# Optimization experiments

Measured on AMD Instinct MI355X. Metric: run time of the kernel, lower is better.

The kernel has to match this reference:

```python
import jax, jax.numpy as jnp
import numpy as np

N, E, B = 50000, 800000, 64
F0, H, C = 8, 2, 64          # node feat dim, heads, per-head out dim
OBS, MH, NA = 128, 256, 16   # obs dim, mlp hidden, n_actions
NEG_SLOPE = 0.2


def setup_inputs() -> dict:
    key = jax.random.key(0)
    ks = jax.random.split(key, 30)
    p = lambda k, shape: (jax.random.normal(k, shape, dtype=jnp.float32) * 0.1)
    inp = {
        "obs": jax.random.normal(ks[0], (B, OBS), dtype=jnp.float32),
        "node_features": jax.random.normal(ks[1], (N, F0), dtype=jnp.float32),
        "edge_index": jax.random.randint(ks[2], (2, E), 0, N, dtype=jnp.int32),
        "batch": jnp.sort(jax.random.randint(ks[3], (N,), 0, B, dtype=jnp.int32)),
        # GAT layer 0: in=F0 -> heads=H, out=C, concat
        "W0": p(ks[4], (F0, H * C)), "a_src0": p(ks[5], (H, C)), "a_dst0": p(ks[6], (H, C)), "b0": p(ks[7], (H * C,)),
        # GAT layer 1: in=H*C -> heads=H, out=C, concat
        "W1": p(ks[8], (H * C, H * C)), "a_src1": p(ks[9], (H, C)), "a_dst1": p(ks[10], (H, C)), "b1": p(ks[11], (H * C,)),
        # GAT layer 2: in=H*C -> heads=1, out=C, no concat
        "W2": p(ks[12], (H * C, C)), "a_src2": p(ks[13], (1, C)), "a_dst2": p(ks[14], (1, C)), "b2": p(ks[15], (C,)),
        # MLP head: combined = C + OBS
        "Ws1": p(ks[16], (C + OBS, MH)), "bs1": p(ks[17], (MH,)),
        "ln_g": jnp.ones((MH,), jnp.float32), "ln_b": jnp.zeros((MH,), jnp.float32),
        "Ws2": p(ks[18], (MH, MH)), "bs2": p(ks[19], (MH,)),
        "Wa": p(ks[20], (MH, NA)), "ba": p(ks[21], (NA,)),
        "Wc": p(ks[22], (MH, 1)), "bc": p(ks[23], (1,)),
    }
    return inp


def gat_layer(x, src, dst, W, a_src, a_dst, bias, heads, out_dim, concat):
    n = x.shape[0]
    h = (x @ W).reshape(n, heads, out_dim)                     # [N,H,C]
    alpha_s = jnp.einsum("nhc,hc->nh", h, a_src)               # [N,H]
    alpha_d = jnp.einsum("nhc,hc->nh", h, a_dst)
    e = jax.nn.leaky_relu(alpha_s[src] + alpha_d[dst], NEG_SLOPE)  # [E,H]
    # scatter-softmax over incoming edges of each dst node (stable)
    emax = jax.ops.segment_max(e, dst, num_segments=n)
    ex = jnp.exp(e - emax[dst])
    denom = jax.ops.segment_sum(ex, dst, num_segments=n)
    alpha = ex / (denom[dst] + 1e-16)                          # [E,H]
    msg = h[src] * alpha[..., None]                            # [E,H,C]
    out = jax.ops.segment_sum(msg, dst, num_segments=n)        # [N,H,C]
    out = out.reshape(n, heads * out_dim) if concat else out.mean(axis=1)
    return out + bias


def reference(obs, node_features, edge_index, batch,
              W0, a_src0, a_dst0, b0, W1, a_src1, a_dst1, b1,
              W2, a_src2, a_dst2, b2,
              Ws1, bs1, ln_g, ln_b, Ws2, bs2, Wa, ba, Wc, bc):
    n = node_features.shape[0]
    # PyG GATConv default add_self_loops=True
    loop = jnp.arange(n, dtype=edge_index.dtype)
    src = jnp.concatenate([edge_index[0], loop])
    dst = jnp.concatenate([edge_index[1], loop])

    x = node_features
    x = jax.nn.elu(gat_layer(x, src, dst, W0, a_src0, a_dst0, b0, H, C, True))
    x = jax.nn.elu(gat_layer(x, src, dst, W1, a_src1, a_dst1, b1, H, C, True))
    x = gat_layer(x, src, dst, W2, a_src2, a_dst2, b2, 1, C, False)

    # global mean pool over graphs
    counts = jax.ops.segment_sum(jnp.ones((n,), x.dtype), batch, num_segments=B)
    pooled = jax.ops.segment_sum(x, batch, num_segments=B) / jnp.maximum(counts, 1.0)[:, None]

    combined = jnp.concatenate([pooled, obs], axis=-1)         # [B, C+OBS]
    h = combined @ Ws1 + bs1
    mu = h.mean(-1, keepdims=True)
    var = ((h - mu) ** 2).mean(-1, keepdims=True)
    h = (h - mu) / jnp.sqrt(var + 1e-5) * ln_g + ln_b
    h = jax.nn.relu(h)
    h = jax.nn.relu(h @ Ws2 + bs2)
    logits = h @ Wa + ba
    value = (h @ Wc + bc).squeeze(-1)
    return logits, value
```

## Files before the change

kernel.cpp:

```cpp
#include <hip/hip_runtime.h>
#include <math.h>


#define LRELU(x) ((x) > 0.f ? (x) : 0.2f * (x))

typedef short bf16x8 __attribute__((ext_vector_type(8)));
typedef unsigned short u16x8 __attribute__((ext_vector_type(8)));
typedef float f32x4 __attribute__((ext_vector_type(4)));
typedef float f32x2 __attribute__((ext_vector_type(2)));

__device__ __forceinline__ float readlane_f(float v, int lane) {
    return __int_as_float(__builtin_amdgcn_readlane(__float_as_int(v), lane));
}
__device__ __forceinline__ unsigned readlane_u(unsigned v, int lane) {
    return (unsigned)__builtin_amdgcn_readlane((int)v, lane);
}
__device__ __forceinline__ unsigned short f2bf(float f) {
    unsigned int u = __float_as_uint(f);
    u = (u + 0x7fffu + ((u >> 16) & 1u)) >> 16;
    return (unsigned short)u;
}
__device__ __forceinline__ float bf2f(unsigned short u) {
    return __uint_as_float((unsigned int)u << 16);
}
__device__ __forceinline__ unsigned char f2fp8(float f) {
    return (unsigned char)(__builtin_amdgcn_cvt_pk_fp8_f32(f, f, 0, false) & 0xff);
}
__device__ __forceinline__ f32x2 fp8pair(unsigned int u) {
    return __builtin_amdgcn_cvt_pk_f32_fp8(u, false);
}


__global__ __launch_bounds__(256) void hist_t0_kernel(
    const int* __restrict__ dst, int* __restrict__ histT,
    int e, int G1, int NB, int n, int hist_blocks, int t0_blocks, int wp_blocks,
    const float* __restrict__ x, const float* __restrict__ W,
    const float* __restrict__ a_src, const float* __restrict__ a_dst,
    unsigned char* __restrict__ h, float* __restrict__ as_o,
    float* __restrict__ ad_o,
    const float* __restrict__ W1, const float* __restrict__ W2,
    unsigned short* __restrict__ Wf1, unsigned short* __restrict__ Wf2,
    const int* __restrict__ batch, int* __restrict__ gstart, int nGraphs) {
    __shared__ unsigned int hist[256];
    __shared__ float xs[2][8][8];
    if ((int)blockIdx.x < hist_blocks) {
        hist[threadIdx.x] = 0;
        __syncthreads();
        int base = blockIdx.x * 2048 + threadIdx.x * 8;
        int d[8];
        if (base + 8 <= e) {
            int4 x0 = *(const int4*)(dst + base);
            int4 x1 = *(const int4*)(dst + base + 4);
            d[0] = x0.x; d[1] = x0.y; d[2] = x0.z; d[3] = x0.w;
            d[4] = x1.x; d[5] = x1.y; d[6] = x1.z; d[7] = x1.w;
        } else {
#pragma unroll
            for (int j = 0; j < 8; j++) {
                int ij = base + j;
                d[j] = (ij < e) ? dst[ij] : -1;
            }
        }
#pragma unroll
        for (int j = 0; j < 8; j++) {
            if (d[j] >= 0) atomicAdd(&hist[d[j] >> 8], 1u);
        }
        __syncthreads();
        int b = threadIdx.x;
        if (b < NB) histT[b * G1 + blockIdx.x] = (int)hist[b];
        return;
    }
    if ((int)blockIdx.x < hist_blocks + t0_blocks) {
        const int bid2 = blockIdx.x - hist_blocks;
        const int tid = threadIdx.x & 127;
        const int half = threadIdx.x >> 7;
        const int node0 = bid2 * 16 + half * 8;

        for (int idx = tid; idx < 64; idx += 128) {
            int ni = idx >> 3, k = idx & 7;
            int ng = node0 + ni;
            xs[half][ni][k] = (ng < n) ? x[(size_t)ng * 8 + k] : 0.f;
        }
        __syncthreads();

        float acc[8];
#pragma unroll
        for (int i = 0; i < 8; i++) acc[i] = 0.f;
#pragma unroll
        for (int k = 0; k < 8; k++) {
            float wk = W[k * 128 + tid];
#pragma unroll
            for (int i = 0; i < 8; i++) acc[i] += xs[half][i][k] * wk;
        }

        const int lane = tid & 63;
        const int head = tid >> 6;
        const int pos = 2 * lane + head;
        const float av = a_src[tid];
        const float dv = a_dst[tid];
#pragma unroll
        for (int i = 0; i < 8; i++) {
            int ng = node0 + i;
            if (ng >= n) break;
            h[(size_t)ng * 128 + pos] = f2fp8(acc[i]);
            float ps = acc[i] * av, pd = acc[i] * dv;
            for (int off = 32; off; off >>= 1) {
                ps += __shfl_xor(ps, off, 64);
                pd += __shfl_xor(pd, off, 64);
            }
            if (lane == 0) {
                as_o[ng * 2 + head] = ps;
                ad_o[ng * 2 + head] = pd;
            }
        }
        return;
    }
    if ((int)blockIdx.x < hist_blocks + t0_blocks + wp_blocks) {
        const int n1 = 8 * 4 * 64;
        const int n2 = 4 * 4 * 64;
        int gid = (blockIdx.x - hist_blocks - t0_blocks) * 256 + threadIdx.x;
        if (gid < n1) {
            int idx = gid;
            int lane = idx & 63, ts = idx >> 6;
            int s = ts & 3, t = ts >> 2;
            int quad = lane >> 4, cn = lane & 15;
#pragma unroll
            for (int j = 0; j < 8; j++)
                Wf1[idx * 8 + j] = f2bf(W1[(s * 32 + quad * 8 + j) * 128 + t * 16 + cn]);
        } else if (gid < n1 + n2) {
            int idx = gid - n1;
            int lane = idx & 63, ts = idx >> 6;
            int s = ts & 3, t = ts >> 2;
            int quad = lane >> 4, cn = lane & 15;
#pragma unroll
            for (int j = 0; j < 8; j++)
                Wf2[idx * 8 + j] = f2bf(W2[(s * 32 + quad * 8 + j) * 64 + t * 16 + cn]);
        }
        return;
    }
    int gid = (blockIdx.x - hist_blocks - t0_blocks - wp_blocks) * 256 + threadIdx.x;
    if (gid < n) {
        int bi = batch[gid];
        if (gid == 0) {
            for (int g = 0; g <= bi; g++) gstart[g] = 0;
        } else {
            int bp = batch[gid - 1];
            if (bi != bp)
                for (int g = bp + 1; g <= bi; g++) gstart[g] = gid;
        }
        if (gid == n - 1) {
            for (int g = bi + 1; g <= nGraphs; g++) gstart[g] = n;
        }
    }
}


__global__ __launch_bounds__(256) void scan2_block_kernel(
    const int* __restrict__ in, int* __restrict__ out,
    int* __restrict__ blockSums, int len) {
    __shared__ int lds[256];
    int t = threadIdx.x;
    int i0 = blockIdx.x * 512 + 2 * t;
    int v0 = (i0 < len) ? in[i0] : 0;
    int v1 = (i0 + 1 < len) ? in[i0 + 1] : 0;
    int s = v0 + v1;
    lds[t] = s;
    __syncthreads();
    for (int off = 1; off < 256; off <<= 1) {
        int u = (t >= off) ? lds[t - off] : 0;
        __syncthreads();
        lds[t] += u;
        __syncthreads();
    }
    int base = lds[t] - s;
    if (i0 < len) out[i0] = base;
    if (i0 + 1 < len) out[i0 + 1] = base + v0;
    if (t == 255) blockSums[blockIdx.x] = lds[255];
}

__global__ __launch_bounds__(256) void scan2_finalize_kernel(
    int* __restrict__ out, const int* __restrict__ blockSums, int len, int nb) {
    __shared__ int lds[256];
    int t = threadIdx.x;
    int v = (t < nb) ? blockSums[t] : 0;
    lds[t] = v;
    __syncthreads();
    for (int off = 1; off < 256; off <<= 1) {
        int u = (t >= off) ? lds[t - off] : 0;
        __syncthreads();
        lds[t] += u;
        __syncthreads();
    }
    const int bid = blockIdx.x;
    const int base = (bid > 0) ? lds[bid - 1] : 0;
    const int total = lds[nb - 1];
    int i0 = bid * 512 + 2 * t;
#pragma unroll
    for (int q = 0; q < 2; q++) {
        int i = i0 + q;
        if (i < len) out[i] += base;
        else if (i == len) out[len] = total;
    }
}


__global__ __launch_bounds__(256) void bucket_scatter_kernel(
    const int* __restrict__ src, const int* __restrict__ dst,
    const int* __restrict__ offs, int* __restrict__ esrc,
    unsigned char* __restrict__ dsub8, int e, int G1) {
    __shared__ unsigned int hist[256];
    hist[threadIdx.x] = 0;
    __syncthreads();
    int base = blockIdx.x * 2048 + threadIdx.x * 8;
    int d[8], s[8];
    if (base + 8 <= e) {
        int4 d0 = *(const int4*)(dst + base);
        int4 d1 = *(const int4*)(dst + base + 4);
        int4 s0 = *(const int4*)(src + base);
        int4 s1 = *(const int4*)(src + base + 4);
        d[0] = d0.x; d[1] = d0.y; d[2] = d0.z; d[3] = d0.w;
        d[4] = d1.x; d[5] = d1.y; d[6] = d1.z; d[7] = d1.w;
        s[0] = s0.x; s[1] = s0.y; s[2] = s0.z; s[3] = s0.w;
        s[4] = s1.x; s[5] = s1.y; s[6] = s1.z; s[7] = s1.w;
    } else {
#pragma unroll
        for (int j = 0; j < 8; j++) {
            int ij = base + j;
            bool v = ij < e;
            d[j] = v ? dst[ij] : -1;
            s[j] = v ? src[ij] : 0;
        }
    }
    unsigned lr[8];
#pragma unroll
    for (int j = 0; j < 8; j++) {
        lr[j] = (d[j] >= 0) ? atomicAdd(&hist[d[j] >> 8], 1u) : 0u;
    }
#pragma unroll
    for (int j = 0; j < 8; j++) {
        if (d[j] >= 0) {
            int pos = offs[(d[j] >> 8) * G1 + blockIdx.x] + (int)lr[j];
            esrc[pos] = s[j];
            dsub8[pos] = (unsigned char)(d[j] & 255);
        }
    }
}


__global__ __launch_bounds__(256) void bucket_csr_kernel(
    const int* __restrict__ offs, const unsigned char* __restrict__ dsub8,
    const int* __restrict__ esrc, int* __restrict__ row_ptr,
    int* __restrict__ col, int G1, int n) {
    __shared__ unsigned int cnt[256];
    __shared__ int rp[256];
    int t = threadIdx.x;
    int b = blockIdx.x;
    cnt[t] = 0;
    __syncthreads();
    int bs = offs[b * G1];
    int be = offs[(b + 1) * G1];
    for (int i = bs + t; i < be; i += 256) {
        atomicAdd(&cnt[dsub8[i]], 1u);
    }
    __syncthreads();
    int v = (int)cnt[t];
    rp[t] = v;
    __syncthreads();
    for (int off = 1; off < 256; off <<= 1) {
        int u = (t >= off) ? rp[t - off] : 0;
        __syncthreads();
        rp[t] += u;
        __syncthreads();
    }
    int excl = rp[t] - v;
    int node = b * 256 + t;
    if (node <= n) row_ptr[node] = bs + excl;
    __syncthreads();
    cnt[t] = (unsigned)excl;
    __syncthreads();
    for (int i = bs + t; i < be; i += 256) {
        int sub = dsub8[i];
        unsigned r = atomicAdd(&cnt[sub], 1u);
        col[bs + (int)r] = esrc[i];
    }
}

template <int OUT, int HEADS>
__device__ __forceinline__ int hpos8(int c) {
    return (HEADS == 2) ? (2 * (c & 63) + (c >> 6)) : c;
}


template <int OUT, int HEADS>
__global__ __launch_bounds__(256) void transform_mfma_kernel(
    const unsigned short* __restrict__ xb, const unsigned short* __restrict__ Wf,
    const float* __restrict__ a_src, const float* __restrict__ a_dst,
    unsigned char* __restrict__ h, float* __restrict__ as_o, float* __restrict__ ad_o,
    int n) {
    constexpr int T = OUT / 16, S = 4;
    const int w = threadIdx.x >> 6, lane = threadIdx.x & 63;
    const int node0 = (blockIdx.x * 4 + w) * 16;
    if (node0 >= n) return;
    const int quad = lane >> 4, col = lane & 15;

    const int arow = node0 + col;
    const bool aok = arow < n;
    bf16x8 a[S];
    const unsigned short* xrow = xb + (size_t)arow * 128 + quad * 8;
#pragma unroll
    for (int s = 0; s < S; s++) {
        bf16x8 z = {0, 0, 0, 0, 0, 0, 0, 0};
        a[s] = aok ? *(const bf16x8*)(xrow + s * 32) : z;
    }

    f32x4 acc[T];
#pragma unroll
    for (int t = 0; t < T; t++) acc[t] = (f32x4){0.f, 0.f, 0.f, 0.f};

#pragma unroll
    for (int s = 0; s < S; s++) {
#pragma unroll
        for (int t = 0; t < T; t++) {
            bf16x8 b = *(const bf16x8*)(Wf + ((size_t)(t * S + s) * 64 + lane) * 8);
            acc[t] = __builtin_amdgcn_mfma_f32_16x16x32_bf16(a[s], b, acc[t], 0, 0, 0);
        }
    }

#pragma unroll
    for (int t = 0; t < T; t++) {
        int pos = hpos8<OUT, HEADS>(t * 16 + col);
#pragma unroll
        for (int r = 0; r < 4; r++) {
            int m = node0 + quad * 4 + r;
            if (m < n) h[(size_t)m * OUT + pos] = f2fp8(acc[t][r]);
        }
    }

#pragma unroll
    for (int r = 0; r < 4; r++) {
        float s0 = 0.f, s1 = 0.f, d0 = 0.f, d1 = 0.f;
#pragma unroll
        for (int t = 0; t < T; t++) {
            float av = a_src[t * 16 + col];
            float dv = a_dst[t * 16 + col];
            float v = acc[t][r];
            if (HEADS == 2 && t >= T / 2) { s1 += v * av; d1 += v * dv; }
            else                          { s0 += v * av; d0 += v * dv; }
        }
        for (int off = 8; off; off >>= 1) {
            s0 += __shfl_xor(s0, off, 64);
            d0 += __shfl_xor(d0, off, 64);
            if (HEADS == 2) {
                s1 += __shfl_xor(s1, off, 64);
                d1 += __shfl_xor(d1, off, 64);
            }
        }
        int m = node0 + quad * 4 + r;
        if (m < n) {
            if (HEADS == 2) {
                if (col == 0)      { as_o[m * 2] = s0;     ad_o[m * 2] = d0; }
                else if (col == 1) { as_o[m * 2 + 1] = s1; ad_o[m * 2 + 1] = d1; }
            } else {
                if (col == 0) { as_o[m] = s0; ad_o[m] = d0; }
            }
        }
    }
}


template <int ACT>
__global__ __launch_bounds__(256) void agg2_kernel(
    const int* __restrict__ row_ptr, const int* __restrict__ col,
    const unsigned char* __restrict__ h, const float2* __restrict__ as2,
    const float2* __restrict__ ad2, const float* __restrict__ bias,
    unsigned short* __restrict__ out, int n) {
    const int node = blockIdx.x * 4 + (threadIdx.x >> 6);
    const int lane = threadIdx.x & 63;
    if (node >= n) return;

    const int beg = row_ptr[node], end = row_ptr[node + 1];
    const float2 adv = ad2[node];
    const unsigned char* __restrict__ hb = h + 2 * lane;

    const float2 avs = as2[node];
    float w0s = __expf(LRELU(avs.x + adv.x));
    float w1s = __expf(LRELU(avs.y + adv.y));
    unsigned int us = *(const unsigned short*)(hb + ((size_t)node << 7));
    f32x2 hvs = fp8pair(us);
    float accL = w0s * hvs.x, accH = w1s * hvs.y;
    float den0 = w0s, den1 = w1s;

    for (int base = beg; base < end; base += 64) {
        int cnt = end - base;
        if (cnt > 64) cnt = 64;
        int s = 0;
        float w0 = 0.f, w1 = 0.f;
        if (lane < cnt) {
            s = col[base + lane];
            float2 av = as2[s];
            w0 = __expf(LRELU(av.x + adv.x));
            w1 = __expf(LRELU(av.y + adv.y));
        }
        float t0 = w0, t1 = w1;
        for (int off = 32; off; off >>= 1) {
            t0 += __shfl_xor(t0, off, 64);
            t1 += __shfl_xor(t1, off, 64);
        }
        den0 += t0;
        den1 += t1;

        unsigned soff = (unsigned)s << 7;
        for (int j = 0; j < cnt; j += 8) {
            unsigned o0 = readlane_u(soff, j);
            unsigned o1 = readlane_u(soff, j + 1);
            unsigned o2 = readlane_u(soff, j + 2);
            unsigned o3 = readlane_u(soff, j + 3);
            unsigned o4 = readlane_u(soff, j + 4);
            unsigned o5 = readlane_u(soff, j + 5);
            unsigned o6 = readlane_u(soff, j + 6);
            unsigned o7 = readlane_u(soff, j + 7);
            unsigned u0 = *(const unsigned short*)(hb + o0);
            unsigned u1 = *(const unsigned short*)(hb + o1);
            unsigned u2 = *(const unsigned short*)(hb + o2);
            unsigned u3 = *(const unsigned short*)(hb + o3);
            unsigned u4 = *(const unsigned short*)(hb + o4);
            unsigned u5 = *(const unsigned short*)(hb + o5);
            unsigned u6 = *(const unsigned short*)(hb + o6);
            unsigned u7 = *(const unsigned short*)(hb + o7);
            float a0 = readlane_f(w0, j),     a1 = readlane_f(w1, j);
            float b0 = readlane_f(w0, j + 1), b1 = readlane_f(w1, j + 1);
            float c0 = readlane_f(w0, j + 2), c1 = readlane_f(w1, j + 2);
            float d0 = readlane_f(w0, j + 3), d1 = readlane_f(w1, j + 3);
            float e0 = readlane_f(w0, j + 4), e1 = readlane_f(w1, j + 4);
            float f0 = readlane_f(w0, j + 5), f1 = readlane_f(w1, j + 5);
            float g0 = readlane_f(w0, j + 6), g1 = readlane_f(w1, j + 6);
            float i0 = readlane_f(w0, j + 7), i1 = readlane_f(w1, j + 7);
            f32x2 hA = fp8pair(u0);
            f32x2 hB = fp8pair(u1);
            f32x2 hC = fp8pair(u2);
            f32x2 hD = fp8pair(u3);
            f32x2 hE = fp8pair(u4);
            f32x2 hF = fp8pair(u5);
            f32x2 hG = fp8pair(u6);
            f32x2 hH = fp8pair(u7);
            accL += a0 * hA.x; accH += a1 * hA.y;
            accL += b0 * hB.x; accH += b1 * hB.y;
            accL += c0 * hC.x; accH += c1 * hC.y;
            accL += d0 * hD.x; accH += d1 * hD.y;
            accL += e0 * hE.x; accH += e1 * hE.y;
            accL += f0 * hF.x; accH += f1 * hF.y;
            accL += g0 * hG.x; accH += g1 * hG.y;
            accL += i0 * hH.x; accH += i1 * hH.y;
        }
    }

    float oL = accL / (den0 + 1e-16f) + bias[lane];
    float oH = accH / (den1 + 1e-16f) + bias[64 + lane];
    if (ACT) {
        oL = oL > 0.f ? oL : expm1f(oL);
        oH = oH > 0.f ? oH : expm1f(oH);
    }
    out[(size_t)node * 128 + lane] = f2bf(oL);
    out[(size_t)node * 128 + 64 + lane] = f2bf(oH);
}


__global__ __launch_bounds__(256) void agg1_kernel(
    const int* __restrict__ row_ptr, const int* __restrict__ col,
    const unsigned char* __restrict__ h, const float* __restrict__ as1,
    const float* __restrict__ ad1, const float* __restrict__ bias,
    unsigned short* __restrict__ out, int n) {
    const int node = blockIdx.x * 4 + (threadIdx.x >> 6);
    const int lane = threadIdx.x & 63;
    if (node >= n) return;

    const int beg = row_ptr[node], end = row_ptr[node + 1];
    const float adv = ad1[node];
    const unsigned char* __restrict__ hb = h + lane;

    float ws = __expf(LRELU(as1[node] + adv));
    float acc = ws * fp8pair((unsigned)hb[(size_t)node << 6]).x;
    float den = ws;

    for (int base = beg; base < end; base += 64) {
        int cnt = end - base;
        if (cnt > 64) cnt = 64;
        int s = 0;
        float w = 0.f;
        if (lane < cnt) {
            s = col[base + lane];
            w = __expf(LRELU(as1[s] + adv));
        }
        float t = w;
        for (int off = 32; off; off >>= 1) t += __shfl_xor(t, off, 64);
        den += t;

        unsigned soff = (unsigned)s << 6;
        for (int j = 0; j < cnt; j += 8) {
            unsigned o0 = readlane_u(soff, j);
            unsigned o1 = readlane_u(soff, j + 1);
            unsigned o2 = readlane_u(soff, j + 2);
            unsigned o3 = readlane_u(soff, j + 3);
            unsigned o4 = readlane_u(soff, j + 4);
            unsigned o5 = readlane_u(soff, j + 5);
            unsigned o6 = readlane_u(soff, j + 6);
            unsigned o7 = readlane_u(soff, j + 7);
            unsigned u0 = hb[o0];
            unsigned u1 = hb[o1];
            unsigned u2 = hb[o2];
            unsigned u3 = hb[o3];
            unsigned u4 = hb[o4];
            unsigned u5 = hb[o5];
            unsigned u6 = hb[o6];
            unsigned u7 = hb[o7];
            float wA = readlane_f(w, j);
            float wB = readlane_f(w, j + 1);
            float wC = readlane_f(w, j + 2);
            float wD = readlane_f(w, j + 3);
            float wE = readlane_f(w, j + 4);
            float wF = readlane_f(w, j + 5);
            float wG = readlane_f(w, j + 6);
            float wH = readlane_f(w, j + 7);
            acc += wA * fp8pair(u0).x;
            acc += wB * fp8pair(u1).x;
            acc += wC * fp8pair(u2).x;
            acc += wD * fp8pair(u3).x;
            acc += wE * fp8pair(u4).x;
            acc += wF * fp8pair(u5).x;
            acc += wG * fp8pair(u6).x;
            acc += wH * fp8pair(u7).x;
        }
    }

    out[(size_t)node * 64 + lane] = f2bf(acc / (den + 1e-16f) + bias[lane]);
}


__global__ __launch_bounds__(512) void mlp_kernel(
    const unsigned short* __restrict__ xbuf, const int* __restrict__ gstart,
    const float* __restrict__ obs,
    const float* __restrict__ Ws1, const float* __restrict__ bs1,
    const float* __restrict__ ln_g, const float* __restrict__ ln_b,
    const float* __restrict__ Ws2, const float* __restrict__ bs2,
    const float* __restrict__ Wa, const float* __restrict__ ba,
    const float* __restrict__ Wc, const float* __restrict__ bc,
    float* __restrict__ out_logits, float* __restrict__ out_value) {
    int b = blockIdx.x;
    int t = threadIdx.x;
    __shared__ float comb[192];
    __shared__ float red[512];
    __shared__ float red2[8][64];
    __shared__ float hs[256];

    const int gs = gstart[b];
    const int ge = gstart[b + 1];

    {
        const int w = t >> 6, lane = t & 63;
        const int rg = w * 8 + (lane >> 3);
        const int sub = lane & 7;
        float acc[8];
#pragma unroll
        for (int j = 0; j < 8; j++) acc[j] = 0.f;
        for (int i = gs + rg; i < ge; i += 64) {
            u16x8 v = *(const u16x8*)(xbuf + (size_t)i * 64 + sub * 8);
#pragma unroll
            for (int j = 0; j < 8; j++) acc[j] += bf2f(v[j]);
        }
#pragma unroll
        for (int off = 8; off <= 32; off <<= 1) {
#pragma unroll
            for (int j = 0; j < 8; j++) acc[j] += __shfl_xor(acc[j], off, 64);
        }
        if (lane < 8) {
#pragma unroll
            for (int j = 0; j < 8; j++) red2[w][lane * 8 + j] = acc[j];
        }
    }
    __syncthreads();
    {
        float cdiv = fmaxf((float)(ge - gs), 1.f);
        if (t < 64) {
            float s = 0.f;
#pragma unroll
            for (int w = 0; w < 8; w++) s += red2[w][t];
            comb[t] = s / cdiv;
        } else if (t < 192) {
            comb[t] = obs[b * 128 + (t - 64)];
        }
    }
    __syncthreads();

    const int t256 = t & 255;
    const int khalf = t >> 8;

    {
        float accA = 0.f, accB = 0.f;
        int k0 = khalf * 96;
#pragma unroll 4
        for (int k = k0; k < k0 + 96; k += 2) {
            accA += comb[k] * Ws1[k * 256 + t256];
            accB += comb[k + 1] * Ws1[(k + 1) * 256 + t256];
        }
        red[t] = accA + accB;
    }
    __syncthreads();
    float acc = 0.f;
    if (t < 256) acc = bs1[t] + red[t] + red[t + 256];
    __syncthreads();

    red[t] = (t < 256) ? acc : 0.f;
    __syncthreads();
    for (int off = 128; off; off >>= 1) {
        if (t < off) red[t] += red[t + off];
        __syncthreads();
    }
    float mu = red[0] / 256.f;
    __syncthreads();
    float d = acc - mu;
    red[t] = (t < 256) ? d * d : 0.f;
    __syncthreads();
    for (int off = 128; off; off >>= 1) {
        if (t < off) red[t] += red[t + off];
        __syncthreads();
    }
    float var = red[0] / 256.f;
    if (t < 256) {
        float hn = d * rsqrtf(var + 1e-5f) * ln_g[t] + ln_b[t];
        hs[t] = hn > 0.f ? hn : 0.f;
    }
    __syncthreads();

    {
        float a2A = 0.f, a2B = 0.f;
        int k0 = khalf * 128;
#pragma unroll 4
        for (int k = k0; k < k0 + 128; k += 2) {
            a2A += hs[k] * Ws2[k * 256 + t256];
            a2B += hs[k + 1] * Ws2[(k + 1) * 256 + t256];
        }
        red[t] = a2A + a2B;
    }
    __syncthreads();
    float acc2 = 0.f;
    if (t < 256) {
        acc2 = bs2[t] + red[t] + red[t + 256];
        acc2 = acc2 > 0.f ? acc2 : 0.f;
    }
    __syncthreads();
    if (t < 256) hs[t] = acc2;
    __syncthreads();

    {
        int o = t & 15, ck = t >> 4;
        float p = 0.f;
#pragma unroll
        for (int k = 0; k < 8; k++)
            p += hs[ck * 8 + k] * Wa[(ck * 8 + k) * 16 + o];
        red[t] = p;
    }
    __syncthreads();
    for (int off = 16; off >= 1; off >>= 1) {
        if ((t >> 4) < off) red[t] += red[t + off * 16];
        __syncthreads();
    }
    if (t < 16) out_logits[b * 16 + t] = red[t] + ba[t];
    __syncthreads();

    red[t] = (t < 256) ? hs[t] * Wc[t] : 0.f;
    __syncthreads();
    for (int off = 256; off; off >>= 1) {
        if (t < off) red[t] += red[t + off];
        __syncthreads();
    }
    if (t == 0) out_value[b] = red[0] + bc[0];
}


extern "C" void kernel_launch(void* const* d_in, const int* in_sizes, int n_in,
                              void* d_out, int out_size, void* d_ws, size_t ws_size,
                              hipStream_t stream) {
    const float* obs    = (const float*)d_in[0];
    const float* nf     = (const float*)d_in[1];
    const int*   ei     = (const int*)d_in[2];
    const int*   batch  = (const int*)d_in[3];
    const float* W0     = (const float*)d_in[4];
    const float* a_src0 = (const float*)d_in[5];
    const float* a_dst0 = (const float*)d_in[6];
    const float* b0     = (const float*)d_in[7];
    const float* W1     = (const float*)d_in[8];
    const float* a_src1 = (const float*)d_in[9];
    const float* a_dst1 = (const float*)d_in[10];
    const float* b1     = (const float*)d_in[11];
    const float* W2     = (const float*)d_in[12];
    const float* a_src2 = (const float*)d_in[13];
    const float* a_dst2 = (const float*)d_in[14];
    const float* b2     = (const float*)d_in[15];
    const float* Ws1    = (const float*)d_in[16];
    const float* bs1    = (const float*)d_in[17];
    const float* ln_g   = (const float*)d_in[18];
    const float* ln_b   = (const float*)d_in[19];
    const float* Ws2    = (const float*)d_in[20];
    const float* bs2    = (const float*)d_in[21];
    const float* Wa     = (const float*)d_in[22];
    const float* ba     = (const float*)d_in[23];
    const float* Wc     = (const float*)d_in[24];
    const float* bc     = (const float*)d_in[25];

    const int N = in_sizes[3];
    const int E = in_sizes[2] / 2;
    const int B = in_sizes[0] / 128;
    const int* src = ei;
    const int* dstp = ei + E;

    char* p = (char*)d_ws;
    auto alloc = [&](size_t bytes) -> void* {
        void* r = (void*)p;
        p += (bytes + 255) & ~(size_t)255;
        return r;
    };
    const int G1 = (E + 2047) / 2048;
    const int NB = (N + 255) >> 8;
    const int L  = NB * G1;
    int*   row_ptr   = (int*)alloc((size_t)(N + 1) * 4);
    int*   col       = (int*)alloc((size_t)E * 4);
    int*   esrc      = (int*)alloc((size_t)E * 4);
    unsigned char* dsub8 = (unsigned char*)alloc((size_t)E);
    int*   histT     = (int*)alloc((size_t)L * 4);
    int*   offs      = (int*)alloc((size_t)(L + 1) * 4);
    unsigned char* hbuf = (unsigned char*)alloc((size_t)N * 128);
    unsigned short* xb = (unsigned short*)alloc((size_t)N * 128 * 2);
    unsigned short* xbuf = (unsigned short*)alloc((size_t)N * 64 * 2);
    float* as_       = (float*)alloc((size_t)N * 2 * 4);
    float* ad_       = (float*)alloc((size_t)N * 2 * 4);
    unsigned short* Wf1 = (unsigned short*)alloc((size_t)8 * 4 * 64 * 8 * 2);
    unsigned short* Wf2 = (unsigned short*)alloc((size_t)4 * 4 * 64 * 8 * 2);
    int* gstart      = (int*)alloc((size_t)(B + 1) * 4);
    int* blockSums = (int*)xb;

    float* out_logits = (float*)d_out;
    float* out_value  = out_logits + (size_t)B * 16;

    int t0_blocks = (N + 15) / 16;
    int wp_blocks = (8 * 4 * 64 + 4 * 4 * 64 + 255) / 256;
    int gb_blocks = (N + 255) / 256;
    hist_t0_kernel<<<G1 + t0_blocks + wp_blocks + gb_blocks, 256, 0, stream>>>(
        dstp, histT, E, G1, NB, N, G1, t0_blocks, wp_blocks,
        nf, W0, a_src0, a_dst0, hbuf, as_, ad_,
        W1, W2, Wf1, Wf2, batch, gstart, B);

    int nbA = (L + 511) / 512;
    scan2_block_kernel<<<nbA, 256, 0, stream>>>(histT, offs, blockSums, L);
    scan2_finalize_kernel<<<(L + 1 + 511) / 512, 256, 0, stream>>>(offs, blockSums, L, nbA);

    bucket_scatter_kernel<<<G1, 256, 0, stream>>>(src, dstp, offs, esrc, dsub8, E, G1);
    bucket_csr_kernel<<<NB, 256, 0, stream>>>(offs, dsub8, esrc, row_ptr, col, G1, N);

    agg2_kernel<1><<<(N + 3) / 4, 256, 0, stream>>>(
        row_ptr, col, hbuf, (const float2*)as_, (const float2*)ad_, b0, xb, N);

    transform_mfma_kernel<128, 2><<<(N + 63) / 64, 256, 0, stream>>>(
        xb, Wf1, a_src1, a_dst1, hbuf, as_, ad_, N);
    agg2_kernel<1><<<(N + 3) / 4, 256, 0, stream>>>(
        row_ptr, col, hbuf, (const float2*)as_, (const float2*)ad_, b1, xb, N);

    transform_mfma_kernel<64, 1><<<(N + 63) / 64, 256, 0, stream>>>(
        xb, Wf2, a_src2, a_dst2, hbuf, as_, ad_, N);
    agg1_kernel<<<(N + 3) / 4, 256, 0, stream>>>(
        row_ptr, col, hbuf, as_, ad_, b2, xbuf, N);

    mlp_kernel<<<B, 512, 0, stream>>>(xbuf, gstart, obs, Ws1, bs1, ln_g, ln_b,
                                      Ws2, bs2, Wa, ba, Wc, bc,
                                      out_logits, out_value);
}
```

Baseline: 292.8 us.

## Process two nodes per wavefront in GAT aggregation with half-wave gathers

Both aggregation kernels now map one node to each 32-lane half of a wavefront instead of a full 64-lane wave. Each lane gathers wider chunks (4 fp8 bytes or 2 bytes), and neighbour offsets and weights go through LDS instead of readlane broadcasts. The intent is to use lanes better, given an average degree of about 16 where most of a 64-wide wave sat idle, and to widen the per-lane loads and stores. The cost is some divergence: both halves loop to the larger of the two degrees, and each chunk adds LDS traffic.

```diff
diff --git a/kernel.cpp b/kernel.cpp
--- a/kernel.cpp
+++ b/kernel.cpp
@@ -9,12 +9,6 @@
 typedef float f32x4 __attribute__((ext_vector_type(4)));
 typedef float f32x2 __attribute__((ext_vector_type(2)));
 
-__device__ __forceinline__ float readlane_f(float v, int lane) {
-    return __int_as_float(__builtin_amdgcn_readlane(__float_as_int(v), lane));
-}
-__device__ __forceinline__ unsigned readlane_u(unsigned v, int lane) {
-    return (unsigned)__builtin_amdgcn_readlane((int)v, lane);
-}
 __device__ __forceinline__ unsigned short f2bf(float f) {
     unsigned int u = __float_as_uint(f);
     u = (u + 0x7fffu + ((u >> 16) & 1u)) >> 16;
@@ -373,94 +367,101 @@
     const unsigned char* __restrict__ h, const float2* __restrict__ as2,
     const float2* __restrict__ ad2, const float* __restrict__ bias,
     unsigned short* __restrict__ out, int n) {
-    const int node = blockIdx.x * 4 + (threadIdx.x >> 6);
+    __shared__ float w0l[4][2][32], w1l[4][2][32];
+    __shared__ unsigned sofl[4][2][32];
+    const int w = threadIdx.x >> 6;
     const int lane = threadIdx.x & 63;
-    if (node >= n) return;
-
-    const int beg = row_ptr[node], end = row_ptr[node + 1];
-    const float2 adv = ad2[node];
-    const unsigned char* __restrict__ hb = h + 2 * lane;
-
-    const float2 avs = as2[node];
-    float w0s = __expf(LRELU(avs.x + adv.x));
-    float w1s = __expf(LRELU(avs.y + adv.y));
-    unsigned int us = *(const unsigned short*)(hb + ((size_t)node << 7));
-    f32x2 hvs = fp8pair(us);
-    float accL = w0s * hvs.x, accH = w1s * hvs.y;
-    float den0 = w0s, den1 = w1s;
-
-    for (int base = beg; base < end; base += 64) {
-        int cnt = end - base;
-        if (cnt > 64) cnt = 64;
-        int s = 0;
+    const int half = lane >> 5, l = lane & 31;
+    const int node = blockIdx.x * 8 + w * 2 + half;
+    const bool active = node < n;
+
+    int beg = 0, deg = 0;
+    float2 adv = make_float2(0.f, 0.f);
+    float den0 = 0.f, den1 = 0.f;
+    float a0 = 0.f, a1 = 0.f, a2 = 0.f, a3 = 0.f;
+    if (active) {
+        beg = row_ptr[node];
+        deg = row_ptr[node + 1] - beg;
+        adv = ad2[node];
+        float2 avs = as2[node];
+        float w0s = __expf(LRELU(avs.x + adv.x));
+        float w1s = __expf(LRELU(avs.y + adv.y));
+        unsigned us = *(const unsigned*)(h + ((size_t)node << 7) + 4 * l);
+        f32x2 p0 = fp8pair(us & 0xffffu);
+        f32x2 p1 = fp8pair(us >> 16);
+        a0 = w0s * p0.x; a1 = w1s * p0.y;
+        a2 = w0s * p1.x; a3 = w1s * p1.y;
+        den0 = w0s; den1 = w1s;
+    }
+    int dmax = deg;
+    for (int off = 32; off; off >>= 1) dmax = max(dmax, __shfl_xor(dmax, off, 64));
+
+    for (int base = 0; base < dmax; base += 32) {
+        int cnt = deg - base;
+        cnt = cnt < 0 ? 0 : (cnt > 32 ? 32 : cnt);
         float w0 = 0.f, w1 = 0.f;
-        if (lane < cnt) {
-            s = col[base + lane];
+        unsigned so = 0;
+        if (l < cnt) {
+            int s = col[beg + base + l];
             float2 av = as2[s];
             w0 = __expf(LRELU(av.x + adv.x));
             w1 = __expf(LRELU(av.y + adv.y));
+            so = (unsigned)s << 7;
         }
         float t0 = w0, t1 = w1;
-        for (int off = 32; off; off >>= 1) {
+        for (int off = 16; off; off >>= 1) {
             t0 += __shfl_xor(t0, off, 64);
             t1 += __shfl_xor(t1, off, 64);
         }
-        den0 += t0;
-        den1 += t1;
-
-        unsigned soff = (unsigned)s << 7;
-        for (int j = 0; j < cnt; j += 8) {
-            unsigned o0 = readlane_u(soff, j);
-            unsigned o1 = readlane_u(soff, j + 1);
-            unsigned o2 = readlane_u(soff, j + 2);
-            unsigned o3 = readlane_u(soff, j + 3);
-            unsigned o4 = readlane_u(soff, j + 4);
-            unsigned o5 = readlane_u(soff, j + 5);
-            unsigned o6 = readlane_u(soff, j + 6);
-            unsigned o7 = readlane_u(soff, j + 7);
-            unsigned u0 = *(const unsigned short*)(hb + o0);
-            unsigned u1 = *(const unsigned short*)(hb + o1);
-            unsigned u2 = *(const unsigned short*)(hb + o2);
-            unsigned u3 = *(const unsigned short*)(hb + o3);
-            unsigned u4 = *(const unsigned short*)(hb + o4);
-            unsigned u5 = *(const unsigned short*)(hb + o5);
-            unsigned u6 = *(const unsigned short*)(hb + o6);
-            unsigned u7 = *(const unsigned short*)(hb + o7);
-            float a0 = readlane_f(w0, j),     a1 = readlane_f(w1, j);
-            float b0 = readlane_f(w0, j + 1), b1 = readlane_f(w1, j + 1);
-            float c0 = readlane_f(w0, j + 2), c1 = readlane_f(w1, j + 2);
-            float d0 = readlane_f(w0, j + 3), d1 = readlane_f(w1, j + 3);
-            float e0 = readlane_f(w0, j + 4), e1 = readlane_f(w1, j + 4);
-            float f0 = readlane_f(w0, j + 5), f1 = readlane_f(w1, j + 5);
-            float g0 = readlane_f(w0, j + 6), g1 = readlane_f(w1, j + 6);
-            float i0 = readlane_f(w0, j + 7), i1 = readlane_f(w1, j + 7);
-            f32x2 hA = fp8pair(u0);
-            f32x2 hB = fp8pair(u1);
-            f32x2 hC = fp8pair(u2);
-            f32x2 hD = fp8pair(u3);
-            f32x2 hE = fp8pair(u4);
-            f32x2 hF = fp8pair(u5);
-            f32x2 hG = fp8pair(u6);
-            f32x2 hH = fp8pair(u7);
-            accL += a0 * hA.x; accH += a1 * hA.y;
-            accL += b0 * hB.x; accH += b1 * hB.y;
-            accL += c0 * hC.x; accH += c1 * hC.y;
-            accL += d0 * hD.x; accH += d1 * hD.y;
-            accL += e0 * hE.x; accH += e1 * hE.y;
-            accL += f0 * hF.x; accH += f1 * hF.y;
-            accL += g0 * hG.x; accH += g1 * hG.y;
-            accL += i0 * hH.x; accH += i1 * hH.y;
-        }
-    }
-
-    float oL = accL / (den0 + 1e-16f) + bias[lane];
-    float oH = accH / (den1 + 1e-16f) + bias[64 + lane];
-    if (ACT) {
-        oL = oL > 0.f ? oL : expm1f(oL);
-        oH = oH > 0.f ? oH : expm1f(oH);
-    }
-    out[(size_t)node * 128 + lane] = f2bf(oL);
-    out[(size_t)node * 128 + 64 + lane] = f2bf(oH);
+        den0 += t0; den1 += t1;
+        w0l[w][half][l] = w0;
+        w1l[w][half][l] = w1;
+        sofl[w][half][l] = so;
+
+        int jmax = dmax - base;
+        jmax = jmax > 32 ? 32 : jmax;
+        for (int j = 0; j < jmax; j += 8) {
+            unsigned u[8];
+#pragma unroll
+            for (int k = 0; k < 8; k++) {
+                unsigned so_k = sofl[w][half][j + k];
+                u[k] = *(const unsigned*)(h + so_k + 4 * l);
+            }
+            float W0[8], W1[8];
+#pragma unroll
+            for (int k = 0; k < 8; k++) {
+                W0[k] = w0l[w][half][j + k];
+                W1[k] = w1l[w][half][j + k];
+            }
+#pragma unroll
+            for (int k = 0; k < 8; k++) {
+                f32x2 p0 = fp8pair(u[k] & 0xffffu);
+                f32x2 p1 = fp8pair(u[k] >> 16);
+                a0 += W0[k] * p0.x; a1 += W1[k] * p0.y;
+                a2 += W0[k] * p1.x; a3 += W1[k] * p1.y;
+            }
+        }
+    }
+
+    if (active) {
+        float2 bA = *(const float2*)(bias + 2 * l);
+        float2 bB = *(const float2*)(bias + 64 + 2 * l);
+        float r0 = 1.f / (den0 + 1e-16f), r1 = 1.f / (den1 + 1e-16f);
+        float o0 = a0 * r0 + bA.x;
+        float o1 = a1 * r1 + bB.x;
+        float o2 = a2 * r0 + bA.y;
+        float o3 = a3 * r1 + bB.y;
+        if (ACT) {
+            o0 = o0 > 0.f ? o0 : expm1f(o0);
+            o1 = o1 > 0.f ? o1 : expm1f(o1);
+            o2 = o2 > 0.f ? o2 : expm1f(o2);
+            o3 = o3 > 0.f ? o3 : expm1f(o3);
+        }
+        unsigned h0 = (unsigned)f2bf(o0) | ((unsigned)f2bf(o2) << 16);
+        unsigned h1 = (unsigned)f2bf(o1) | ((unsigned)f2bf(o3) << 16);
+        *(unsigned*)(out + (size_t)node * 128 + 2 * l) = h0;
+        *(unsigned*)(out + (size_t)node * 128 + 64 + 2 * l) = h1;
+    }
 }
 
 
@@ -469,69 +470,75 @@
     const unsigned char* __restrict__ h, const float* __restrict__ as1,
     const float* __restrict__ ad1, const float* __restrict__ bias,
     unsigned short* __restrict__ out, int n) {
-    const int node = blockIdx.x * 4 + (threadIdx.x >> 6);
+    __shared__ float wl[4][2][32];
+    __shared__ unsigned sofl[4][2][32];
+    const int w = threadIdx.x >> 6;
     const int lane = threadIdx.x & 63;
-    if (node >= n) return;
-
-    const int beg = row_ptr[node], end = row_ptr[node + 1];
-    const float adv = ad1[node];
-    const unsigned char* __restrict__ hb = h + lane;
-
-    float ws = __expf(LRELU(as1[node] + adv));
-    float acc = ws * fp8pair((unsigned)hb[(size_t)node << 6]).x;
-    float den = ws;
-
-    for (int base = beg; base < end; base += 64) {
-        int cnt = end - base;
-        if (cnt > 64) cnt = 64;
-        int s = 0;
-        float w = 0.f;
-        if (lane < cnt) {
-            s = col[base + lane];
-            w = __expf(LRELU(as1[s] + adv));
-        }
-        float t = w;
-        for (int off = 32; off; off >>= 1) t += __shfl_xor(t, off, 64);
+    const int half = lane >> 5, l = lane & 31;
+    const int node = blockIdx.x * 8 + w * 2 + half;
+    const bool active = node < n;
+
+    int beg = 0, deg = 0;
+    float adv = 0.f, den = 0.f, a0 = 0.f, a2 = 0.f;
+    if (active) {
+        beg = row_ptr[node];
+        deg = row_ptr[node + 1] - beg;
+        adv = ad1[node];
+        float ws = __expf(LRELU(as1[node] + adv));
+        unsigned us = *(const unsigned short*)(h + ((size_t)node << 6) + 2 * l);
+        f32x2 p = fp8pair(us);
+        a0 = ws * p.x;
+        a2 = ws * p.y;
+        den = ws;
+    }
+    int dmax = deg;
+    for (int off = 32; off; off >>= 1) dmax = max(dmax, __shfl_xor(dmax, off, 64));
+
+    for (int base = 0; base < dmax; base += 32) {
+        int cnt = deg - base;
+        cnt = cnt < 0 ? 0 : (cnt > 32 ? 32 : cnt);
+        float w0 = 0.f;
+        unsigned so = 0;
+        if (l < cnt) {
+            int s = col[beg + base + l];
+            w0 = __expf(LRELU(as1[s] + adv));
+            so = (unsigned)s << 6;
+        }
+        float t = w0;
+        for (int off = 16; off; off >>= 1) t += __shfl_xor(t, off, 64);
         den += t;
-
-        unsigned soff = (unsigned)s << 6;
-        for (int j = 0; j < cnt; j += 8) {
-            unsigned o0 = readlane_u(soff, j);
-            unsigned o1 = readlane_u(soff, j + 1);
-            unsigned o2 = readlane_u(soff, j + 2);
-            unsigned o3 = readlane_u(soff, j + 3);
-            unsigned o4 = readlane_u(soff, j + 4);
-            unsigned o5 = readlane_u(soff, j + 5);
-            unsigned o6 = readlane_u(soff, j + 6);
-            unsigned o7 = readlane_u(soff, j + 7);
-            unsigned u0 = hb[o0];
-            unsigned u1 = hb[o1];
-            unsigned u2 = hb[o2];
-            unsigned u3 = hb[o3];
-            unsigned u4 = hb[o4];
-            unsigned u5 = hb[o5];
-            unsigned u6 = hb[o6];
-            unsigned u7 = hb[o7];
-            float wA = readlane_f(w, j);
-            float wB = readlane_f(w, j + 1);
-            float wC = readlane_f(w, j + 2);
-            float wD = readlane_f(w, j + 3);
-            float wE = readlane_f(w, j + 4);
-            float wF = readlane_f(w, j + 5);
-            float wG = readlane_f(w, j + 6);
-            float wH = readlane_f(w, j + 7);
-            acc += wA * fp8pair(u0).x;
-            acc += wB * fp8pair(u1).x;
-            acc += wC * fp8pair(u2).x;
-            acc += wD * fp8pair(u3).x;
-            acc += wE * fp8pair(u4).x;
-            acc += wF * fp8pair(u5).x;
-            acc += wG * fp8pair(u6).x;
-            acc += wH * fp8pair(u7).x;
-        }
-    }
-
-    out[(size_t)node * 64 + lane] = f2bf(acc / (den + 1e-16f) + bias[lane]);
+        wl[w][half][l] = w0;
+        sofl[w][half][l] = so;
+
+        int jmax = dmax - base;
+        jmax = jmax > 32 ? 32 : jmax;
+        for (int j = 0; j < jmax; j += 8) {
+            unsigned u[8];
+#pragma unroll
+            for (int k = 0; k < 8; k++) {
+                unsigned so_k = sofl[w][half][j + k];
+                u[k] = *(const unsigned short*)(h + so_k + 2 * l);
+            }
+            float W0[8];
+#pragma unroll
+            for (int k = 0; k < 8; k++) W0[k] = wl[w][half][j + k];
+#pragma unroll
+            for (int k = 0; k < 8; k++) {
+                f32x2 p = fp8pair(u[k]);
+                a0 += W0[k] * p.x;
+                a2 += W0[k] * p.y;
+            }
+        }
+    }
+
+    if (active) {
+        float2 bA = *(const float2*)(bias + 2 * l);
+        float r = 1.f / (den + 1e-16f);
+        float o0 = a0 * r + bA.x;
+        float o2 = a2 * r + bA.y;
+        unsigned hv = (unsigned)f2bf(o0) | ((unsigned)f2bf(o2) << 16);
+        *(unsigned*)(out + (size_t)node * 64 + 2 * l) = hv;
+    }
 }
 
 
@@ -755,17 +762,17 @@
     bucket_scatter_kernel<<<G1, 256, 0, stream>>>(src, dstp, offs, esrc, dsub8, E, G1);
     bucket_csr_kernel<<<NB, 256, 0, stream>>>(offs, dsub8, esrc, row_ptr, col, G1, N);
 
-    agg2_kernel<1><<<(N + 3) / 4, 256, 0, stream>>>(
+    agg2_kernel<1><<<(N + 7) / 8, 256, 0, stream>>>(
         row_ptr, col, hbuf, (const float2*)as_, (const float2*)ad_, b0, xb, N);
 
     transform_mfma_kernel<128, 2><<<(N + 63) / 64, 256, 0, stream>>>(
         xb, Wf1, a_src1, a_dst1, hbuf, as_, ad_, N);
-    agg2_kernel<1><<<(N + 3) / 4, 256, 0, stream>>>(
+    agg2_kernel<1><<<(N + 7) / 8, 256, 0, stream>>>(
         row_ptr, col, hbuf, (const float2*)as_, (const float2*)ad_, b1, xb, N);
 
     transform_mfma_kernel<64, 1><<<(N + 63) / 64, 256, 0, stream>>>(
         xb, Wf2, a_src2, a_dst2, hbuf, as_, ad_, N);
-    agg1_kernel<<<(N + 3) / 4, 256, 0, stream>>>(
+    agg1_kernel<<<(N + 7) / 8, 256, 0, stream>>>(
         row_ptr, col, hbuf, as_, ad_, b2, xbuf, N);
 
     mlp_kernel<<<B, 512, 0, stream>>>(xbuf, gstart, obs, Ws1, bs1, ln_g, ln_b,
```

After: 265.5 us. -9.4%, faster.
